# Kernel optimization log

Hardware: AMD Instinct MI355X
Metric: run time of the kernel (lower is better)

## Reference

```python
import jax, jax.numpy as jnp
import numpy as np

N, E = 100000, 1600000
IN_C, HID_C, OUT_C = 128, 64, 40


def setup_inputs() -> dict:
    key = jax.random.key(0)
    ks = jax.random.split(key, 8)
    s = lambda fan_in: 1.0 / np.sqrt(fan_in)
    return {
        "x": jax.random.normal(ks[0], (N, IN_C), dtype=jnp.float32),
        "edge_index": jax.random.randint(ks[1], (2, E), 0, N, dtype=jnp.int64),
        # SAGEConv layer 1: lin_l (on aggregated neighbors, with bias) + lin_r (root, no bias)
        "W_l1": jax.random.uniform(ks[2], (IN_C, HID_C), jnp.float32, -s(IN_C), s(IN_C)),
        "b_l1": jnp.zeros((HID_C,), jnp.float32),
        "W_r1": jax.random.uniform(ks[3], (IN_C, HID_C), jnp.float32, -s(IN_C), s(IN_C)),
        # SAGEConv layer 2
        "W_l2": jax.random.uniform(ks[4], (HID_C, OUT_C), jnp.float32, -s(HID_C), s(HID_C)),
        "b_l2": jnp.zeros((OUT_C,), jnp.float32),
        "W_r2": jax.random.uniform(ks[5], (HID_C, OUT_C), jnp.float32, -s(HID_C), s(HID_C)),
    }


def _sage_conv(x, src, dst, W_l, b_l, W_r, n_nodes):
    # mean-aggregate neighbor features: scatter-add x[src] onto dst, divide by degree
    agg = jax.ops.segment_sum(x[src], dst, num_segments=n_nodes)  # [N, F]
    deg = jax.ops.segment_sum(jnp.ones((src.shape[0],), x.dtype), dst, num_segments=n_nodes)
    mean = agg / jnp.maximum(deg, 1.0)[:, None]
    return mean @ W_l + b_l + x @ W_r


def reference(x, edge_index, W_l1, b_l1, W_r1, W_l2, b_l2, W_r2):
    src, dst = edge_index[0], edge_index[1]  # messages flow src -> dst
    # eval mode: dropout is identity
    hid = _sage_conv(x, src, dst, W_l1, b_l1, W_r1, N)
    hid = jax.nn.relu(hid)
    out = _sage_conv(hid, src, dst, W_l2, b_l2, W_r2, N)
    return jax.nn.log_softmax(out, axis=1)
```

## Files before the change

kernel.cpp:

```cpp
#include <hip/hip_runtime.h>
#include <hip/hip_bf16.h>

#define N_NODES 100000
#define E_EDGES 1600000
#define IN_C 128
#define HID_C 64
#define OUT_C 40

#define NBUCK 196
#define BCAP 9216
#define B1_EPT 16
#define B1_CHUNK (256 * B1_EPT)
#define B1_GRID ((E_EDGES + B1_CHUNK - 1) / B1_CHUNK)
#define GEMM1_GRID ((N_NODES + 63) / 64)

typedef unsigned short ushort_t;
typedef unsigned int uint_t;
typedef unsigned char uchar_t;
typedef __attribute__((ext_vector_type(8))) short bf16x8;
typedef __attribute__((ext_vector_type(4))) float f32x4;
typedef __attribute__((ext_vector_type(2))) float f32x2;

__device__ __forceinline__ float bfu2f(ushort_t u) {
    return __uint_as_float(((uint_t)u) << 16);
}
__device__ __forceinline__ ushort_t f2bfu(float f) {
    uint_t u = __float_as_uint(f);
    return (ushort_t)((u + 0x7FFFu + ((u >> 16) & 1u)) >> 16);
}
__device__ __forceinline__ uchar_t f2fp8(float f) {
    int p = __builtin_amdgcn_cvt_pk_fp8_f32(f, f, 0, false);
    return (uchar_t)(p & 0xff);
}

__global__ __launch_bounds__(256) void k_prep(const int* __restrict__ src, const int* __restrict__ dst,
                                              int* __restrict__ bcur, int* __restrict__ bucket,
                                              const float* __restrict__ Wl1, const float* __restrict__ Wr1,
                                              const float* __restrict__ Wl2, const float* __restrict__ Wr2,
                                              ushort_t* __restrict__ Wt1, ushort_t* __restrict__ Wt2) {
    __shared__ int cnt[NBUCK];
    __shared__ int base[NBUCK];
    const int t = threadIdx.x;

    if (blockIdx.x < B1_GRID) {
        const int e0 = blockIdx.x * B1_CHUNK;
        for (int i = t; i < NBUCK; i += 256) cnt[i] = 0;
        __syncthreads();

        int myp[B1_EPT];
        int myb[B1_EPT];
#pragma unroll
        for (int j = 0; j < B1_EPT; ++j) {
            int e = e0 + t + j * 256;
            if (e < E_EDGES) {
                int d = dst[e];
                myp[j] = src[e] | ((d & 511) << 17);
                myb[j] = d >> 9;
                atomicAdd(&cnt[myb[j]], 1);
            } else {
                myb[j] = -1;
            }
        }
        __syncthreads();
        for (int i = t; i < NBUCK; i += 256) {
            base[i] = atomicAdd(&bcur[i], cnt[i]);
            cnt[i] = 0;
        }
        __syncthreads();
#pragma unroll
        for (int j = 0; j < B1_EPT; ++j) {
            if (myb[j] >= 0) {
                int b = myb[j];
                int loc = atomicAdd(&cnt[b], 1);
                int pos = base[b] + loc;
                if (pos < BCAP) bucket[(size_t)b * BCAP + pos] = myp[j];
            }
        }
    } else {
        int i = (blockIdx.x - B1_GRID) * 256 + t;
        if (i < 128 * 128) {
            int n = i >> 7, k = i & 127;
            float v = (n < 64) ? Wl1[k * 64 + n] : Wr1[k * 64 + (n - 64)];
            Wt1[n * 128 + k] = f2bfu(v);
        }
        if (i < 80 * 64) {
            int n = i >> 6, k = i & 63;
            float v = (n < 40) ? Wl2[k * 40 + n] : Wr2[k * 40 + (n - 40)];
            Wt2[n * 64 + k] = f2bfu(v);
        }
    }
}

struct SmemCsr {
    int red[256];
    int hist[512];
    int sc[2][512];
    int cur[512];
    int csrbuf[BCAP];
};
struct SmemGemm1 {
    ushort_t xs[64 * 136];
    ushort_t wsm[128 * 136];
};
union SmemK2 {
    SmemCsr c;
    SmemGemm1 g;
};

__global__ __launch_bounds__(256) void k_csr_gemm1(const int* __restrict__ bucket, const int* __restrict__ bcur,
                                                   int* __restrict__ rowptr, int* __restrict__ csr,
                                                   const float* __restrict__ x, const ushort_t* __restrict__ Wt,
                                                   uchar_t* __restrict__ h1l, ushort_t* __restrict__ h1r) {
    __shared__ SmemK2 sm;
    const int t = threadIdx.x;

    if (blockIdx.x < NBUCK) {
        const int b = blockIdx.x;
        const int n0 = b << 9;
        const int nb = min(512, N_NODES - n0);
        const int sz = min(bcur[b], BCAP);
        const int* bdata = bucket + (size_t)b * BCAP;

        int v = (t < b) ? min(bcur[t], BCAP) : 0;
        sm.c.red[t] = v;
        __syncthreads();
        for (int off = 128; off > 0; off >>= 1) {
            if (t < off) sm.c.red[t] += sm.c.red[t + off];
            __syncthreads();
        }
        const int cbase = sm.c.red[0];

        for (int i = t; i < 512; i += 256) sm.c.hist[i] = 0;
        __syncthreads();
        for (int i = t; i < sz; i += 256) {
            int p = bdata[i];
            atomicAdd(&sm.c.hist[p >> 17], 1);
        }
        __syncthreads();
        for (int i = t; i < 512; i += 256) sm.c.sc[0][i] = sm.c.hist[i];
        __syncthreads();
        int pp = 0;
        for (int off = 1; off < 512; off <<= 1) {
            for (int i = t; i < 512; i += 256)
                sm.c.sc[1 - pp][i] = sm.c.sc[pp][i] + ((i >= off) ? sm.c.sc[pp][i - off] : 0);
            __syncthreads();
            pp ^= 1;
        }
        for (int i = t; i < 512; i += 256) {
            int exc = sm.c.sc[pp][i] - sm.c.hist[i];
            sm.c.cur[i] = exc;
            if (i < nb) rowptr[n0 + i] = cbase + exc;
        }
        __syncthreads();
        for (int i = t; i < sz; i += 256) {
            int p = bdata[i];
            int pos = atomicAdd(&sm.c.cur[p >> 17], 1);
            sm.c.csrbuf[pos] = p & 0x1FFFF;
        }
        __syncthreads();
        for (int i = t; i < sz; i += 256)
            csr[cbase + i] = sm.c.csrbuf[i];
        if (b == NBUCK - 1 && t == 0) rowptr[N_NODES] = cbase + sz;
    } else {
        const int row_base = (blockIdx.x - NBUCK) * 64;

        for (int i = t; i < 128 * 16; i += 256) {
            int n = i >> 4, seg = i & 15;
            uint4 v = *(const uint4*)(Wt + n * 128 + seg * 8);
            *(uint4*)(sm.g.wsm + n * 136 + seg * 8) = v;
        }
        for (int i = t; i < 64 * 32; i += 256) {
            int row = i >> 5, seg = i & 31;
            int gr = row_base + row;
            float4 v = make_float4(0.f, 0.f, 0.f, 0.f);
            if (gr < N_NODES) v = *(const float4*)(x + (size_t)gr * IN_C + seg * 4);
            ushort4 u;
            u.x = f2bfu(v.x); u.y = f2bfu(v.y); u.z = f2bfu(v.z); u.w = f2bfu(v.w);
            *(ushort4*)(sm.g.xs + row * 136 + seg * 4) = u;
        }
        __syncthreads();

        const int wv = t >> 6, lane = t & 63;
        const int m = lane & 15, quad = lane >> 4;
        const int m0 = wv * 16;

        bf16x8 a[4];
#pragma unroll
        for (int kk = 0; kk < 4; ++kk)
            a[kk] = *(const bf16x8*)(sm.g.xs + (m0 + m) * 136 + kk * 32 + quad * 8);

        f32x4 acc[8];
#pragma unroll
        for (int nt = 0; nt < 8; ++nt) acc[nt] = (f32x4){0.f, 0.f, 0.f, 0.f};

#pragma unroll
        for (int nt = 0; nt < 8; ++nt) {
#pragma unroll
            for (int kk = 0; kk < 4; ++kk) {
                bf16x8 b = *(const bf16x8*)(sm.g.wsm + (nt * 16 + m) * 136 + kk * 32 + quad * 8);
                acc[nt] = __builtin_amdgcn_mfma_f32_16x16x32_bf16(a[kk], b, acc[nt], 0, 0, 0);
            }
        }

        const int grow_base = row_base + m0 + quad * 4;
#pragma unroll
        for (int r = 0; r < 4; ++r) {
            int grow = grow_base + r;
            if (grow < N_NODES) {
#pragma unroll
                for (int nt = 0; nt < 4; ++nt)
                    h1l[(size_t)grow * HID_C + nt * 16 + m] = f2fp8(acc[nt][r]);
#pragma unroll
                for (int nt = 4; nt < 8; ++nt)
                    h1r[(size_t)grow * HID_C + (nt - 4) * 16 + m] = f2bfu(acc[nt][r]);
            }
        }
    }
}

__global__ __launch_bounds__(256) void k_agg1(const int* __restrict__ rowptr, const int* __restrict__ csr,
                                              const uchar_t* __restrict__ h1l, const ushort_t* __restrict__ h1r,
                                              const float* __restrict__ b1, ushort_t* __restrict__ hid) {
    int row = (blockIdx.x * 256 + threadIdx.x) >> 6;
    int lane = threadIdx.x & 63;
    if (row >= N_NODES) return;
    int start = rowptr[row];
    int end = rowptr[row + 1];
    const int slot = lane >> 3;
    const int part = lane & 7;
    f32x2 acc[4];
#pragma unroll
    for (int j = 0; j < 4; ++j) acc[j] = (f32x2){0.f, 0.f};

    int base = start;
    for (; base + 8 <= end; base += 8) {
        int s = csr[base + slot];
        uint2 u = *(const uint2*)(h1l + ((size_t)s << 6) + part * 8);
        acc[0] += __builtin_amdgcn_cvt_pk_f32_fp8(u.x, false);
        acc[1] += __builtin_amdgcn_cvt_pk_f32_fp8(u.x, true);
        acc[2] += __builtin_amdgcn_cvt_pk_f32_fp8(u.y, false);
        acc[3] += __builtin_amdgcn_cvt_pk_f32_fp8(u.y, true);
    }
    if (base < end) {
        int e = base + slot;
        int s = csr[min(e, end - 1)];
        uint2 u = *(const uint2*)(h1l + ((size_t)s << 6) + part * 8);
        if (e >= end) { u.x = 0u; u.y = 0u; }
        acc[0] += __builtin_amdgcn_cvt_pk_f32_fp8(u.x, false);
        acc[1] += __builtin_amdgcn_cvt_pk_f32_fp8(u.x, true);
        acc[2] += __builtin_amdgcn_cvt_pk_f32_fp8(u.y, false);
        acc[3] += __builtin_amdgcn_cvt_pk_f32_fp8(u.y, true);
    }
#pragma unroll
    for (int off = 8; off <= 32; off <<= 1) {
#pragma unroll
        for (int j = 0; j < 4; ++j) {
            f32x2 tt;
            tt.x = __shfl_xor(acc[j].x, off);
            tt.y = __shfl_xor(acc[j].y, off);
            acc[j] += tt;
        }
    }

    if (slot == 0) {
        float inv = __builtin_amdgcn_rcpf(fmaxf((float)(end - start), 1.0f));
        size_t bi = (size_t)row * HID_C + part * 8;
        ushort_t rr[8];
        *(uint4*)rr = *(const uint4*)(h1r + bi);
        float4 bb0 = *(const float4*)(b1 + part * 8);
        float4 bb1 = *(const float4*)(b1 + part * 8 + 4);
        ushort_t o[8];
        o[0] = f2bfu(fmaxf(acc[0].x * inv + bfu2f(rr[0]) + bb0.x, 0.f));
        o[1] = f2bfu(fmaxf(acc[0].y * inv + bfu2f(rr[1]) + bb0.y, 0.f));
        o[2] = f2bfu(fmaxf(acc[1].x * inv + bfu2f(rr[2]) + bb0.z, 0.f));
        o[3] = f2bfu(fmaxf(acc[1].y * inv + bfu2f(rr[3]) + bb0.w, 0.f));
        o[4] = f2bfu(fmaxf(acc[2].x * inv + bfu2f(rr[4]) + bb1.x, 0.f));
        o[5] = f2bfu(fmaxf(acc[2].y * inv + bfu2f(rr[5]) + bb1.y, 0.f));
        o[6] = f2bfu(fmaxf(acc[3].x * inv + bfu2f(rr[6]) + bb1.z, 0.f));
        o[7] = f2bfu(fmaxf(acc[3].y * inv + bfu2f(rr[7]) + bb1.w, 0.f));
        *(uint4*)(hid + bi) = *(const uint4*)o;
    }
}

__global__ __launch_bounds__(256) void k_gemm2(const ushort_t* __restrict__ hid,
                                               const ushort_t* __restrict__ Wt,
                                               uchar_t* __restrict__ h2l,
                                               ushort_t* __restrict__ h2r) {
    __shared__ ushort_t hs[64 * 72];
    __shared__ ushort_t wsm[80 * 72];
    const int t = threadIdx.x;
    const int row_base = blockIdx.x * 64;

    for (int i = t; i < 80 * 8; i += 256) {
        int n = i >> 3, seg = i & 7;
        uint4 v = *(const uint4*)(Wt + n * 64 + seg * 8);
        *(uint4*)(wsm + n * 72 + seg * 8) = v;
    }
    for (int i = t; i < 64 * 8; i += 256) {
        int row = i >> 3, seg = i & 7;
        int gr = row_base + row;
        uint4 v = make_uint4(0u, 0u, 0u, 0u);
        if (gr < N_NODES) v = *(const uint4*)(hid + (size_t)gr * HID_C + seg * 8);
        *(uint4*)(hs + row * 72 + seg * 8) = v;
    }
    __syncthreads();

    const int wv = t >> 6, lane = t & 63;
    const int m = lane & 15, quad = lane >> 4;
    const int m0 = wv * 16;

    bf16x8 a[2];
#pragma unroll
    for (int kk = 0; kk < 2; ++kk)
        a[kk] = *(const bf16x8*)(hs + (m0 + m) * 72 + kk * 32 + quad * 8);

    f32x4 acc[5];
#pragma unroll
    for (int nt = 0; nt < 5; ++nt) acc[nt] = (f32x4){0.f, 0.f, 0.f, 0.f};

#pragma unroll
    for (int nt = 0; nt < 5; ++nt) {
#pragma unroll
        for (int kk = 0; kk < 2; ++kk) {
            bf16x8 b = *(const bf16x8*)(wsm + (nt * 16 + m) * 72 + kk * 32 + quad * 8);
            acc[nt] = __builtin_amdgcn_mfma_f32_16x16x32_bf16(a[kk], b, acc[nt], 0, 0, 0);
        }
    }

    const int grow_base = row_base + m0 + quad * 4;
#pragma unroll
    for (int r = 0; r < 4; ++r) {
        int grow = grow_base + r;
        if (grow < N_NODES) {
#pragma unroll
            for (int nt = 0; nt < 5; ++nt) {
                int col = nt * 16 + m;
                float v = acc[nt][r];
                if (col < OUT_C) h2l[(size_t)grow * 64 + col] = f2fp8(v);
                else             h2r[(size_t)grow * OUT_C + (col - OUT_C)] = f2bfu(v);
            }
        }
    }
}

__global__ __launch_bounds__(256) void k_agg2(const int* __restrict__ rowptr, const int* __restrict__ csr,
                                              const uchar_t* __restrict__ h2l, const ushort_t* __restrict__ h2r,
                                              const float* __restrict__ b2, float* __restrict__ out) {
    int row = (blockIdx.x * 256 + threadIdx.x) >> 6;
    int lane = threadIdx.x & 63;
    if (row >= N_NODES) return;
    int start = rowptr[row];
    int end = rowptr[row + 1];
    const int slot = lane >> 3;
    const int part = lane & 7;
    f32x2 acc[4];
#pragma unroll
    for (int j = 0; j < 4; ++j) acc[j] = (f32x2){0.f, 0.f};

    int base = start;
    for (; base + 8 <= end; base += 8) {
        int s = csr[base + slot];
        uint2 u = *(const uint2*)(h2l + ((size_t)s << 6) + part * 8);
        acc[0] += __builtin_amdgcn_cvt_pk_f32_fp8(u.x, false);
        acc[1] += __builtin_amdgcn_cvt_pk_f32_fp8(u.x, true);
        acc[2] += __builtin_amdgcn_cvt_pk_f32_fp8(u.y, false);
        acc[3] += __builtin_amdgcn_cvt_pk_f32_fp8(u.y, true);
    }
    if (base < end) {
        int e = base + slot;
        int s = csr[min(e, end - 1)];
        uint2 u = *(const uint2*)(h2l + ((size_t)s << 6) + part * 8);
        if (e >= end) { u.x = 0u; u.y = 0u; }
        acc[0] += __builtin_amdgcn_cvt_pk_f32_fp8(u.x, false);
        acc[1] += __builtin_amdgcn_cvt_pk_f32_fp8(u.x, true);
        acc[2] += __builtin_amdgcn_cvt_pk_f32_fp8(u.y, false);
        acc[3] += __builtin_amdgcn_cvt_pk_f32_fp8(u.y, true);
    }
#pragma unroll
    for (int off = 8; off <= 32; off <<= 1) {
#pragma unroll
        for (int j = 0; j < 4; ++j) {
            f32x2 tt;
            tt.x = __shfl_xor(acc[j].x, off);
            tt.y = __shfl_xor(acc[j].y, off);
            acc[j] += tt;
        }
    }

    const bool fin = (slot == 0) && (part < 5);
    float inv = __builtin_amdgcn_rcpf(fmaxf((float)(end - start), 1.0f));
    f32x2 v2[4];
    if (fin) {
        size_t bi = (size_t)row * OUT_C + part * 8;
        ushort_t rr[8];
        *(uint2*)&rr[0] = *(const uint2*)(h2r + bi);
        *(uint2*)&rr[4] = *(const uint2*)(h2r + bi + 4);
        float4 bb0 = *(const float4*)(b2 + part * 8);
        float4 bb1 = *(const float4*)(b2 + part * 8 + 4);
        v2[0] = (f32x2){acc[0].x * inv + bfu2f(rr[0]) + bb0.x, acc[0].y * inv + bfu2f(rr[1]) + bb0.y};
        v2[1] = (f32x2){acc[1].x * inv + bfu2f(rr[2]) + bb0.z, acc[1].y * inv + bfu2f(rr[3]) + bb0.w};
        v2[2] = (f32x2){acc[2].x * inv + bfu2f(rr[4]) + bb1.x, acc[2].y * inv + bfu2f(rr[5]) + bb1.y};
        v2[3] = (f32x2){acc[3].x * inv + bfu2f(rr[6]) + bb1.z, acc[3].y * inv + bfu2f(rr[7]) + bb1.w};
    } else {
#pragma unroll
        for (int j = 0; j < 4; ++j) v2[j] = (f32x2){-1e30f, -1e30f};
    }
    f32x2 m2;
    m2.x = fmaxf(fmaxf(v2[0].x, v2[1].x), fmaxf(v2[2].x, v2[3].x));
    m2.y = fmaxf(fmaxf(v2[0].y, v2[1].y), fmaxf(v2[2].y, v2[3].y));
    float pm = fmaxf(m2.x, m2.y);
#pragma unroll
    for (int off = 1; off <= 4; off <<= 1) pm = fmaxf(pm, __shfl_xor(pm, off));
    float es = 0.f;
#pragma unroll
    for (int j = 0; j < 4; ++j) {
        es += __expf(v2[j].x - pm);
        es += __expf(v2[j].y - pm);
    }
#pragma unroll
    for (int off = 1; off <= 4; off <<= 1) es += __shfl_xor(es, off);
    float ls = __logf(es);
    if (fin) {
        size_t bo = (size_t)row * OUT_C + part * 8;
        *(float4*)(out + bo) = make_float4(v2[0].x - pm - ls, v2[0].y - pm - ls,
                                           v2[1].x - pm - ls, v2[1].y - pm - ls);
        *(float4*)(out + bo + 4) = make_float4(v2[2].x - pm - ls, v2[2].y - pm - ls,
                                               v2[3].x - pm - ls, v2[3].y - pm - ls);
    }
}

extern "C" void kernel_launch(void* const* d_in, const int* in_sizes, int n_in,
                              void* d_out, int out_size, void* d_ws, size_t ws_size,
                              hipStream_t stream) {
    const float* x   = (const float*)d_in[0];
    const int*   ei  = (const int*)d_in[1];
    const float* Wl1 = (const float*)d_in[2];
    const float* b1  = (const float*)d_in[3];
    const float* Wr1 = (const float*)d_in[4];
    const float* Wl2 = (const float*)d_in[5];
    const float* b2  = (const float*)d_in[6];
    const float* Wr2 = (const float*)d_in[7];

    size_t u = 0;
    int*      bucket = (int*)d_ws;             u += (size_t)NBUCK * BCAP;
    int*      bcur   = (int*)d_ws + u;         u += NBUCK + 4;
    int*      rowptr = (int*)d_ws + u;         u += N_NODES + 1;
    int*      csr    = (int*)d_ws + u;         u += E_EDGES;
    u = (u + 3) & ~(size_t)3;
    ushort_t* Wt1    = (ushort_t*)((int*)d_ws + u); u += 128 * 128 / 2;
    ushort_t* Wt2    = (ushort_t*)((int*)d_ws + u); u += 80 * 64 / 2;
    uchar_t*  h1l    = (uchar_t*)((int*)d_ws + u);  u += (size_t)N_NODES * HID_C / 4;
    ushort_t* h1r    = (ushort_t*)((int*)d_ws + u); u += (size_t)N_NODES * HID_C / 2;
    ushort_t* hid    = (ushort_t*)((int*)d_ws + u); u += (size_t)N_NODES * HID_C / 2;
    uchar_t*  h2l    = (uchar_t*)((int*)d_ws + u);  u += (size_t)N_NODES * 64 / 4;
    ushort_t* h2r    = (ushort_t*)((int*)d_ws + u); u += (size_t)N_NODES * OUT_C / 2;
    if (ws_size < u * 4) return;

    hipMemsetAsync(bcur, 0, NBUCK * sizeof(int), stream);

    const int* src = ei;
    const int* dst = ei + E_EDGES;

    k_prep<<<B1_GRID + 64, 256, 0, stream>>>(src, dst, bcur, bucket, Wl1, Wr1, Wl2, Wr2, Wt1, Wt2);
    k_csr_gemm1<<<NBUCK + GEMM1_GRID, 256, 0, stream>>>(bucket, bcur, rowptr, csr, x, Wt1, h1l, h1r);
    k_agg1<<<N_NODES / 4, 256, 0, stream>>>(rowptr, csr, h1l, h1r, b1, hid);
    k_gemm2<<<GEMM1_GRID, 256, 0, stream>>>(hid, Wt2, h2l, h2r);
    k_agg2<<<N_NODES / 4, 256, 0, stream>>>(rowptr, csr, h2l, h2r, b2, (float*)d_out);
}
```

Measured before the change: 257.8 us.

## Fuse layer-1 aggregation into layer-2 GEMM and pre-shift CSR indices

Merges the layer-1 mean aggregation with the layer-2 GEMM: each 64-row block now aggregates its own rows into shared memory and runs the MFMA GEMM directly, so the bf16 hidden tensor is never written to or re-read from global memory and one launch is removed. CSR entries now store source index times 64, which removes the shift in both gather loops, and rowptr is read as one int2. In exchange the aggregation runs on only 1563 blocks, each wave looping serially over 16 rows, which may hurt latency hiding and occupancy compared with the earlier one-row-per-wave grid.

```diff
diff --git a/kernel.cpp b/kernel.cpp
--- a/kernel.cpp
+++ b/kernel.cpp
@@ -12,7 +12,7 @@
 #define B1_EPT 16
 #define B1_CHUNK (256 * B1_EPT)
 #define B1_GRID ((E_EDGES + B1_CHUNK - 1) / B1_CHUNK)
-#define GEMM1_GRID ((N_NODES + 63) / 64)
+#define TILE_GRID ((N_NODES + 63) / 64)
 
 typedef unsigned short ushort_t;
 typedef unsigned int uint_t;
@@ -155,7 +155,7 @@
         for (int i = t; i < sz; i += 256) {
             int p = bdata[i];
             int pos = atomicAdd(&sm.c.cur[p >> 17], 1);
-            sm.c.csrbuf[pos] = p & 0x1FFFF;
+            sm.c.csrbuf[pos] = (p & 0x1FFFF) << 6;
         }
         __syncthreads();
         for (int i = t; i < sz; i += 256)
@@ -218,94 +218,90 @@
     }
 }
 
-__global__ __launch_bounds__(256) void k_agg1(const int* __restrict__ rowptr, const int* __restrict__ csr,
-                                              const uchar_t* __restrict__ h1l, const ushort_t* __restrict__ h1r,
-                                              const float* __restrict__ b1, ushort_t* __restrict__ hid) {
-    int row = (blockIdx.x * 256 + threadIdx.x) >> 6;
-    int lane = threadIdx.x & 63;
-    if (row >= N_NODES) return;
-    int start = rowptr[row];
-    int end = rowptr[row + 1];
-    const int slot = lane >> 3;
-    const int part = lane & 7;
-    f32x2 acc[4];
-#pragma unroll
-    for (int j = 0; j < 4; ++j) acc[j] = (f32x2){0.f, 0.f};
-
-    int base = start;
-    for (; base + 8 <= end; base += 8) {
-        int s = csr[base + slot];
-        uint2 u = *(const uint2*)(h1l + ((size_t)s << 6) + part * 8);
-        acc[0] += __builtin_amdgcn_cvt_pk_f32_fp8(u.x, false);
-        acc[1] += __builtin_amdgcn_cvt_pk_f32_fp8(u.x, true);
-        acc[2] += __builtin_amdgcn_cvt_pk_f32_fp8(u.y, false);
-        acc[3] += __builtin_amdgcn_cvt_pk_f32_fp8(u.y, true);
-    }
-    if (base < end) {
-        int e = base + slot;
-        int s = csr[min(e, end - 1)];
-        uint2 u = *(const uint2*)(h1l + ((size_t)s << 6) + part * 8);
-        if (e >= end) { u.x = 0u; u.y = 0u; }
-        acc[0] += __builtin_amdgcn_cvt_pk_f32_fp8(u.x, false);
-        acc[1] += __builtin_amdgcn_cvt_pk_f32_fp8(u.x, true);
-        acc[2] += __builtin_amdgcn_cvt_pk_f32_fp8(u.y, false);
-        acc[3] += __builtin_amdgcn_cvt_pk_f32_fp8(u.y, true);
-    }
-#pragma unroll
-    for (int off = 8; off <= 32; off <<= 1) {
-#pragma unroll
-        for (int j = 0; j < 4; ++j) {
-            f32x2 tt;
-            tt.x = __shfl_xor(acc[j].x, off);
-            tt.y = __shfl_xor(acc[j].y, off);
-            acc[j] += tt;
-        }
-    }
-
-    if (slot == 0) {
-        float inv = __builtin_amdgcn_rcpf(fmaxf((float)(end - start), 1.0f));
-        size_t bi = (size_t)row * HID_C + part * 8;
-        ushort_t rr[8];
-        *(uint4*)rr = *(const uint4*)(h1r + bi);
-        float4 bb0 = *(const float4*)(b1 + part * 8);
-        float4 bb1 = *(const float4*)(b1 + part * 8 + 4);
-        ushort_t o[8];
-        o[0] = f2bfu(fmaxf(acc[0].x * inv + bfu2f(rr[0]) + bb0.x, 0.f));
-        o[1] = f2bfu(fmaxf(acc[0].y * inv + bfu2f(rr[1]) + bb0.y, 0.f));
-        o[2] = f2bfu(fmaxf(acc[1].x * inv + bfu2f(rr[2]) + bb0.z, 0.f));
-        o[3] = f2bfu(fmaxf(acc[1].y * inv + bfu2f(rr[3]) + bb0.w, 0.f));
-        o[4] = f2bfu(fmaxf(acc[2].x * inv + bfu2f(rr[4]) + bb1.x, 0.f));
-        o[5] = f2bfu(fmaxf(acc[2].y * inv + bfu2f(rr[5]) + bb1.y, 0.f));
-        o[6] = f2bfu(fmaxf(acc[3].x * inv + bfu2f(rr[6]) + bb1.z, 0.f));
-        o[7] = f2bfu(fmaxf(acc[3].y * inv + bfu2f(rr[7]) + bb1.w, 0.f));
-        *(uint4*)(hid + bi) = *(const uint4*)o;
-    }
-}
-
-__global__ __launch_bounds__(256) void k_gemm2(const ushort_t* __restrict__ hid,
-                                               const ushort_t* __restrict__ Wt,
-                                               uchar_t* __restrict__ h2l,
-                                               ushort_t* __restrict__ h2r) {
+__global__ __launch_bounds__(256) void k_agg1_gemm2(const int* __restrict__ rowptr, const int* __restrict__ csr,
+                                                    const uchar_t* __restrict__ h1l, const ushort_t* __restrict__ h1r,
+                                                    const float* __restrict__ b1, const ushort_t* __restrict__ Wt,
+                                                    uchar_t* __restrict__ h2l, ushort_t* __restrict__ h2r) {
     __shared__ ushort_t hs[64 * 72];
     __shared__ ushort_t wsm[80 * 72];
     const int t = threadIdx.x;
     const int row_base = blockIdx.x * 64;
+    const int wv = t >> 6, lane = t & 63;
+    const int slot = lane >> 3;
+    const int part = lane & 7;
 
     for (int i = t; i < 80 * 8; i += 256) {
         int n = i >> 3, seg = i & 7;
         uint4 v = *(const uint4*)(Wt + n * 64 + seg * 8);
         *(uint4*)(wsm + n * 72 + seg * 8) = v;
     }
-    for (int i = t; i < 64 * 8; i += 256) {
-        int row = i >> 3, seg = i & 7;
-        int gr = row_base + row;
-        uint4 v = make_uint4(0u, 0u, 0u, 0u);
-        if (gr < N_NODES) v = *(const uint4*)(hid + (size_t)gr * HID_C + seg * 8);
-        *(uint4*)(hs + row * 72 + seg * 8) = v;
+
+    float4 bb0, bb1;
+    if (slot == 0) {
+        bb0 = *(const float4*)(b1 + part * 8);
+        bb1 = *(const float4*)(b1 + part * 8 + 4);
+    }
+    for (int r16 = 0; r16 < 16; ++r16) {
+        int lrow = wv * 16 + r16;
+        int row = row_base + lrow;
+        if (row < N_NODES) {
+            int2 rp = *(const int2*)(rowptr + row);
+            int start = rp.x, end = rp.y;
+            f32x2 acc[4];
+#pragma unroll
+            for (int j = 0; j < 4; ++j) acc[j] = (f32x2){0.f, 0.f};
+
+            int base = start;
+            for (; base + 8 <= end; base += 8) {
+                int s = csr[base + slot];
+                uint2 u = *(const uint2*)(h1l + s + part * 8);
+                acc[0] += __builtin_amdgcn_cvt_pk_f32_fp8(u.x, false);
+                acc[1] += __builtin_amdgcn_cvt_pk_f32_fp8(u.x, true);
+                acc[2] += __builtin_amdgcn_cvt_pk_f32_fp8(u.y, false);
+                acc[3] += __builtin_amdgcn_cvt_pk_f32_fp8(u.y, true);
+            }
+            if (base < end) {
+                int e = base + slot;
+                int s = csr[min(e, end - 1)];
+                uint2 u = *(const uint2*)(h1l + s + part * 8);
+                if (e >= end) { u.x = 0u; u.y = 0u; }
+                acc[0] += __builtin_amdgcn_cvt_pk_f32_fp8(u.x, false);
+                acc[1] += __builtin_amdgcn_cvt_pk_f32_fp8(u.x, true);
+                acc[2] += __builtin_amdgcn_cvt_pk_f32_fp8(u.y, false);
+                acc[3] += __builtin_amdgcn_cvt_pk_f32_fp8(u.y, true);
+            }
+#pragma unroll
+            for (int off = 8; off <= 32; off <<= 1) {
+#pragma unroll
+                for (int j = 0; j < 4; ++j) {
+                    f32x2 tt;
+                    tt.x = __shfl_xor(acc[j].x, off);
+                    tt.y = __shfl_xor(acc[j].y, off);
+                    acc[j] += tt;
+                }
+            }
+            if (slot == 0) {
+                float inv = __builtin_amdgcn_rcpf(fmaxf((float)(end - start), 1.0f));
+                ushort_t rr[8];
+                *(uint4*)rr = *(const uint4*)(h1r + (size_t)row * HID_C + part * 8);
+                ushort_t o[8];
+                o[0] = f2bfu(fmaxf(acc[0].x * inv + bfu2f(rr[0]) + bb0.x, 0.f));
+                o[1] = f2bfu(fmaxf(acc[0].y * inv + bfu2f(rr[1]) + bb0.y, 0.f));
+                o[2] = f2bfu(fmaxf(acc[1].x * inv + bfu2f(rr[2]) + bb0.z, 0.f));
+                o[3] = f2bfu(fmaxf(acc[1].y * inv + bfu2f(rr[3]) + bb0.w, 0.f));
+                o[4] = f2bfu(fmaxf(acc[2].x * inv + bfu2f(rr[4]) + bb1.x, 0.f));
+                o[5] = f2bfu(fmaxf(acc[2].y * inv + bfu2f(rr[5]) + bb1.y, 0.f));
+                o[6] = f2bfu(fmaxf(acc[3].x * inv + bfu2f(rr[6]) + bb1.z, 0.f));
+                o[7] = f2bfu(fmaxf(acc[3].y * inv + bfu2f(rr[7]) + bb1.w, 0.f));
+                *(uint4*)(hs + lrow * 72 + part * 8) = *(const uint4*)o;
+            }
+        } else if (slot == 0) {
+            uint4 z = make_uint4(0u, 0u, 0u, 0u);
+            *(uint4*)(hs + lrow * 72 + part * 8) = z;
+        }
     }
     __syncthreads();
 
-    const int wv = t >> 6, lane = t & 63;
     const int m = lane & 15, quad = lane >> 4;
     const int m0 = wv * 16;
 
@@ -349,8 +345,8 @@
     int row = (blockIdx.x * 256 + threadIdx.x) >> 6;
     int lane = threadIdx.x & 63;
     if (row >= N_NODES) return;
-    int start = rowptr[row];
-    int end = rowptr[row + 1];
+    int2 rp = *(const int2*)(rowptr + row);
+    int start = rp.x, end = rp.y;
     const int slot = lane >> 3;
     const int part = lane & 7;
     f32x2 acc[4];
@@ -360,7 +356,7 @@
     int base = start;
     for (; base + 8 <= end; base += 8) {
         int s = csr[base + slot];
-        uint2 u = *(const uint2*)(h2l + ((size_t)s << 6) + part * 8);
+        uint2 u = *(const uint2*)(h2l + s + part * 8);
         acc[0] += __builtin_amdgcn_cvt_pk_f32_fp8(u.x, false);
         acc[1] += __builtin_amdgcn_cvt_pk_f32_fp8(u.x, true);
         acc[2] += __builtin_amdgcn_cvt_pk_f32_fp8(u.y, false);
@@ -369,7 +365,7 @@
     if (base < end) {
         int e = base + slot;
         int s = csr[min(e, end - 1)];
-        uint2 u = *(const uint2*)(h2l + ((size_t)s << 6) + part * 8);
+        uint2 u = *(const uint2*)(h2l + s + part * 8);
         if (e >= end) { u.x = 0u; u.y = 0u; }
         acc[0] += __builtin_amdgcn_cvt_pk_f32_fp8(u.x, false);
         acc[1] += __builtin_amdgcn_cvt_pk_f32_fp8(u.x, true);
@@ -451,7 +447,6 @@
     ushort_t* Wt2    = (ushort_t*)((int*)d_ws + u); u += 80 * 64 / 2;
     uchar_t*  h1l    = (uchar_t*)((int*)d_ws + u);  u += (size_t)N_NODES * HID_C / 4;
     ushort_t* h1r    = (ushort_t*)((int*)d_ws + u); u += (size_t)N_NODES * HID_C / 2;
-    ushort_t* hid    = (ushort_t*)((int*)d_ws + u); u += (size_t)N_NODES * HID_C / 2;
     uchar_t*  h2l    = (uchar_t*)((int*)d_ws + u);  u += (size_t)N_NODES * 64 / 4;
     ushort_t* h2r    = (ushort_t*)((int*)d_ws + u); u += (size_t)N_NODES * OUT_C / 2;
     if (ws_size < u * 4) return;
@@ -462,8 +457,7 @@
     const int* dst = ei + E_EDGES;
 
     k_prep<<<B1_GRID + 64, 256, 0, stream>>>(src, dst, bcur, bucket, Wl1, Wr1, Wl2, Wr2, Wt1, Wt2);
-    k_csr_gemm1<<<NBUCK + GEMM1_GRID, 256, 0, stream>>>(bucket, bcur, rowptr, csr, x, Wt1, h1l, h1r);
-    k_agg1<<<N_NODES / 4, 256, 0, stream>>>(rowptr, csr, h1l, h1r, b1, hid);
-    k_gemm2<<<GEMM1_GRID, 256, 0, stream>>>(hid, Wt2, h2l, h2r);
+    k_csr_gemm1<<<NBUCK + TILE_GRID, 256, 0, stream>>>(bucket, bcur, rowptr, csr, x, Wt1, h1l, h1r);
+    k_agg1_gemm2<<<TILE_GRID, 256, 0, stream>>>(rowptr, csr, h1l, h1r, b1, Wt2, h2l, h2r);
     k_agg2<<<N_NODES / 4, 256, 0, stream>>>(rowptr, csr, h2l, h2r, b2, (float*)d_out);
 }
```

Measured after the change: 257.0 us. No clear change (-0.3%).
